# Optimization experiments

Hardware: AMD Instinct MI355X
Metric: run time of the kernel (lower is better)

## Reference

```python
import jax, jax.numpy as jnp
import numpy as np

N, P, S, ENT = 256, 4, 40, 60
E = 1 + P + S + ENT          # 105 graph nodes (query + paras + sents + ents)
D = 1024                     # input_dim == hidden_dim
H, T = 8, 3                  # gnn heads, edge types
DH = D // H                  # per-head output dim
NEG = -1e30


def setup_inputs() -> dict:
    key = jax.random.key(0)
    ks = jax.random.split(key, 12)
    f = lambda k, sh, s: jax.random.normal(k, sh, jnp.float32) * s
    return {
        "query_vec": f(ks[0], (N, D), 1.0),
        "para_state": f(ks[1], (N, P, D), 1.0),
        "sent_state": f(ks[2], (N, S, D), 1.0),
        "ent_state": f(ks[3], (N, ENT, D), 1.0),
        "para_mask": jax.random.randint(ks[4], (N, P), 0, 2).astype(jnp.float32),
        "sent_mask": jax.random.randint(ks[5], (N, S), 0, 2).astype(jnp.float32),
        "ent_mask": jax.random.randint(ks[6], (N, ENT), 0, 2).astype(jnp.float32),
        "adj": jax.random.randint(ks[7], (N, E, E), 0, T + 1).astype(jnp.int32),
        "W": f(ks[8], (H, T, D, DH), 0.05),        # per head/edge-type projection
        "a": f(ks[9], (H, T, 2 * DH), 0.05),       # GAT attention vector [a1;a2]
        "qW1": f(ks[10], (H, T, D, 2 * DH), 0.05), # query-gate layer 1
        "qW2": f(ks[11], (H, T, 2 * DH, 2 * DH), 0.05),  # query-gate layer 2
    }


def _graph_block(x, query_vec, node_mask, adj, W, a, qW1, qW2):
    # x: [N,E,D], node_mask: [N,E,1], adj: [N,E,E] int (0 = no edge, 1..T = edge type)
    # per head/edge-type projections: [H,T,N,E,DH]
    h = jnp.einsum('ned,htdk->htnek', x, W)
    # query-conditioned gate (q_attn=True): sigmoid(relu(q @ W1) @ W2) -> [H,T,N,2DH]
    g = jax.nn.sigmoid(jnp.einsum('htnk,htkm->htnm',
                                  jax.nn.relu(jnp.einsum('nd,htdk->htnk', query_vec, qW1)),
                                  qW2))
    # decomposed GAT score: score[i,j] = lrelu((g1*h_i)@a1 + (g2*h_j)@a2)
    a1, a2 = a[..., :DH], a[..., DH:]
    f1 = jnp.einsum('htnek,htnk->htne', h, g[..., :DH] * a1[:, :, None, :])
    f2 = jnp.einsum('htnek,htnk->htne', h, g[..., DH:] * a2[:, :, None, :])
    score = jax.nn.leaky_relu(f1[..., :, None] + f2[..., None, :], 0.2)  # [H,T,N,E,E]
    # accumulate only where adj matches the edge type (i+1)
    etype = (jnp.arange(T, dtype=adj.dtype) + 1)[None, :, None, None, None]
    scores = jnp.sum(jnp.where(adj[None, None] == etype, score, 0.0), axis=1)  # [H,N,E,E]
    scores = jnp.where(adj[None] > 0, scores, NEG)
    coefs = jax.nn.softmax(scores, axis=-1)                 # [H,N,E,E]
    # original uses the last edge-type projection, node-masked, for aggregation
    h_last = h[:, -1] * node_mask[None]                     # [H,N,E,DH]
    out = jnp.einsum('hnij,hnjd->hnid', coefs, h_last)      # [H,N,E,DH]
    out = jnp.transpose(out, (1, 2, 0, 3)).reshape(x.shape[0], E, H * DH)
    out = jax.nn.relu(out)                                  # dropout p=0 in eval
    return out + x                                          # residual (identity align)


def reference(query_vec, para_state, sent_state, ent_state,
              para_mask, sent_mask, ent_mask, adj, W, a, qW1, qW2):
    x = jnp.concatenate([query_vec[:, None, :], para_state, sent_state, ent_state], axis=1)  # [N,E,D]
    node_mask = jnp.concatenate(
        [jnp.ones((x.shape[0], 1), x.dtype), para_mask, sent_mask, ent_mask], axis=-1)[..., None]  # [N,E,1]
    graph_state = _graph_block(x, query_vec, node_mask, adj, W, a, qW1, qW2)  # [N,E,D]
    return graph_state
```

## Files before the change

kernel.cpp:

```cpp
#include <hip/hip_runtime.h>
#include <stdint.h>


typedef unsigned short u16;
typedef __bf16 bf16;
typedef __bf16 bf16x8 __attribute__((ext_vector_type(8)));
typedef float f32x4 __attribute__((ext_vector_type(4)));

#define N_ 256
#define E_ 105
#define D_ 1024
#define H_ 8
#define DH_ 128
#define NE_ 26880

__device__ __forceinline__ u16 f2b(float f) { bf16 h = (bf16)f; return __builtin_bit_cast(u16, h); }
__device__ __forceinline__ float b2f(u16 u) { bf16 h = __builtin_bit_cast(bf16, u); return (float)h; }

#define AS1 __attribute__((address_space(1)))
#define AS3 __attribute__((address_space(3)))

__device__ __forceinline__ void load16_lds(const void* g, void* l) {
  __builtin_amdgcn_global_load_lds((AS1 void*)(unsigned long long)(uintptr_t)g,
                                   (AS3 void*)l, 16, 0, 0);
}

__device__ __forceinline__ void gemm128(u16* lds, const u16* A, const u16* B, int K,
                                        int lda, int ldb, f32x4 (&acc)[4][4]) {
  u16* lA = lds;
  u16* lB = lds + 8192;
  const int tid  = threadIdx.x;
  const int lane = tid & 63;
  const int wave = tid >> 6;
  const int ln15 = lane & 15;
  const int lq   = lane >> 4;
  const int wRow = (wave >> 1) * 64;
  const int wCol = (wave & 1) * 64;

  const int iters = K >> 6;
  for (int kt = 0; kt < iters; ++kt) {
    const char* Ab = (const char*)A + kt * 128;
    const char* Bb = (const char*)B + kt * 128;
#pragma unroll
    for (int m = 0; m < 4; ++m) {
      int ci  = m * 256 + tid;
      int row = ci >> 3;
      int g   = (ci & 7) ^ (row & 7);
      char* dstA = (char*)lA + m * 4096 + wave * 1024;
      char* dstB = (char*)lB + m * 4096 + wave * 1024;
      load16_lds(Ab + (long)row * ((long)lda * 2) + g * 16, dstA);
      load16_lds(Bb + (long)row * ((long)ldb * 2) + g * 16, dstB);
    }
    __syncthreads();
#pragma unroll
    for (int ks = 0; ks < 2; ++ks) {
      const int cc = ks * 4 + lq;
      bf16x8 af[4], bfv[4];
#pragma unroll
      for (int i = 0; i < 4; ++i) {
        int r = wRow + i * 16 + ln15;
        af[i] = *(const bf16x8*)&lA[r * 64 + ((cc ^ (r & 7)) << 3)];
        int c = wCol + i * 16 + ln15;
        bfv[i] = *(const bf16x8*)&lB[c * 64 + ((cc ^ (c & 7)) << 3)];
      }
#pragma unroll
      for (int i = 0; i < 4; ++i)
#pragma unroll
        for (int j = 0; j < 4; ++j)
          acc[i][j] = __builtin_amdgcn_mfma_f32_16x16x32_bf16(af[i], bfv[j], acc[i][j], 0, 0, 0);
    }
    __syncthreads();
  }
}

__device__ __forceinline__ void zero_acc(f32x4 (&acc)[4][4]) {
  f32x4 z = {0.f, 0.f, 0.f, 0.f};
#pragma unroll
  for (int i = 0; i < 4; ++i)
#pragma unroll
    for (int j = 0; j < 4; ++j) acc[i][j] = z;
}

__global__ __launch_bounds__(256) void k_cast(const float* src, u16* dst, long n) {
  long i = ((long)blockIdx.x * 256 + threadIdx.x) * 4;
  if (i >= n) return;
  float4 v = *(const float4*)(src + i);
  ushort4 o;
  o.x = f2b(v.x); o.y = f2b(v.y); o.z = f2b(v.z); o.w = f2b(v.w);
  *(ushort4*)(dst + i) = o;
}

__global__ __launch_bounds__(256) void k_build(const float* q, const float* para,
                                               const float* sent, const float* ent,
                                               const float* pm, const float* sm,
                                               const float* em, u16* x, float* nmask) {
  long idx = (long)blockIdx.x * 256 + threadIdx.x;
  if (idx >= (long)NE_ * 128) return;
  int ne = (int)(idx >> 7), dc = (int)(idx & 127);
  int n = ne / E_, e = ne - n * E_;
  const float* src;
  if (e == 0)      src = q + (long)n * D_;
  else if (e < 5)  src = para + (long)(n * 4 + (e - 1)) * D_;
  else if (e < 45) src = sent + (long)(n * 40 + (e - 5)) * D_;
  else             src = ent + (long)(n * 60 + (e - 45)) * D_;
  float4 v0 = *(const float4*)(src + dc * 8);
  float4 v1 = *(const float4*)(src + dc * 8 + 4);
  uint4 o;
  o.x = (unsigned)f2b(v0.x) | ((unsigned)f2b(v0.y) << 16);
  o.y = (unsigned)f2b(v0.z) | ((unsigned)f2b(v0.w) << 16);
  o.z = (unsigned)f2b(v1.x) | ((unsigned)f2b(v1.y) << 16);
  o.w = (unsigned)f2b(v1.z) | ((unsigned)f2b(v1.w) << 16);
  *(uint4*)(x + (long)ne * D_ + dc * 8) = o;
  if (dc == 0) {
    float mv;
    if (e == 0)      mv = 1.f;
    else if (e < 5)  mv = pm[n * 4 + e - 1];
    else if (e < 45) mv = sm[n * 40 + e - 5];
    else             mv = em[n * 60 + e - 45];
    nmask[ne] = mv;
  }
}

__global__ __launch_bounds__(256) void k_tr(const float* src, u16* dst, int R, int C,
                                            long sStr, long dStr) {
  __shared__ u16 t[32][33];
  const int bz = blockIdx.y;
  const int tilesC = C >> 5;
  const int tr = (blockIdx.x / tilesC) << 5;
  const int tc = (blockIdx.x % tilesC) << 5;
  const int lr = threadIdx.x >> 5;
  const int lc = threadIdx.x & 31;
#pragma unroll
  for (int i = 0; i < 4; ++i)
    t[lr + i * 8][lc] = f2b(src[bz * sStr + (long)(tr + lr + i * 8) * C + tc + lc]);
  __syncthreads();
#pragma unroll
  for (int i = 0; i < 4; ++i)
    dst[bz * dStr + (long)(tc + lr + i * 8) * R + tr + lc] = t[lc][lr + i * 8];
}

__global__ __launch_bounds__(256) void k_qw1(const u16* x, const u16* qW1t, u16* r_bf) {
  __shared__ u16 shm[16384];
  const int bx = blockIdx.x;
  const int ht = bx >> 2, nt = (bx >> 1) & 1, mt = bx & 1;
  f32x4 acc[4][4];
  zero_acc(acc);
  gemm128(shm, x + (long)nt * 128 * (E_ * D_), qW1t + ((long)ht * 256 + mt * 128) * D_,
          1024, E_ * D_, 1024, acc);
  const int tid = threadIdx.x, lane = tid & 63, wave = tid >> 6;
  const int ln15 = lane & 15, lq = lane >> 4;
  const int wRow = (wave >> 1) * 64, wCol = (wave & 1) * 64;
#pragma unroll
  for (int rt = 0; rt < 4; ++rt)
#pragma unroll
    for (int ct = 0; ct < 4; ++ct)
#pragma unroll
      for (int rg = 0; rg < 4; ++rg) {
        int n = nt * 128 + wRow + rt * 16 + lq * 4 + rg;
        int m = mt * 128 + wCol + ct * 16 + ln15;
        float v = acc[rt][ct][rg];
        if (v < 0.f) v = 0.f;
        r_bf[((long)ht * 256 + n) * 256 + m] = f2b(v);
      }
}

__global__ __launch_bounds__(256) void k_qw2(const u16* r_bf, const u16* qW2t, const float* a,
                                             u16* ga) {
  __shared__ u16 shm[16384];
  const int bx = blockIdx.x;
  const int ht = bx >> 2, nt = (bx >> 1) & 1, mt = bx & 1;
  f32x4 acc[4][4];
  zero_acc(acc);
  gemm128(shm, r_bf + ((long)ht * 256 + nt * 128) * 256, qW2t + ((long)ht * 256 + mt * 128) * 256,
          256, 256, 256, acc);
  const int tid = threadIdx.x, lane = tid & 63, wave = tid >> 6;
  const int ln15 = lane & 15, lq = lane >> 4;
  const int wRow = (wave >> 1) * 64, wCol = (wave & 1) * 64;
#pragma unroll
  for (int rt = 0; rt < 4; ++rt)
#pragma unroll
    for (int ct = 0; ct < 4; ++ct)
#pragma unroll
      for (int rg = 0; rg < 4; ++rg) {
        int n = nt * 128 + wRow + rt * 16 + lq * 4 + rg;
        int m = mt * 128 + wCol + ct * 16 + ln15;
        float v = acc[rt][ct][rg];
        float sig = 1.f / (1.f + __expf(-v));
        float gv = sig * a[ht * 256 + m];
        int s = m >> 7, kk = m & 127;
        ga[(((long)ht * 2 + s) * 256 + n) * 128 + kk] = f2b(gv);
      }
}

__global__ __launch_bounds__(256) void k_w12(const u16* ga, const u16* Wb, u16* w12) {
  __shared__ u16 shm[16384];
  const int bx = blockIdx.x;
  const int c = bx >> 4, r2 = bx & 15;
  const int nt = r2 >> 3, dt = r2 & 7;
  const int ht = c >> 1;
  f32x4 acc[4][4];
  zero_acc(acc);
  gemm128(shm, ga + ((long)c * 256 + nt * 128) * 128, Wb + (long)ht * 131072 + dt * 128 * 128,
          128, 128, 128, acc);
  const int tid = threadIdx.x, lane = tid & 63, wave = tid >> 6;
  const int ln15 = lane & 15, lq = lane >> 4;
  const int wRow = (wave >> 1) * 64, wCol = (wave & 1) * 64;
#pragma unroll
  for (int rt = 0; rt < 4; ++rt)
#pragma unroll
    for (int ct = 0; ct < 4; ++ct)
#pragma unroll
      for (int rg = 0; rg < 4; ++rg) {
        int n = nt * 128 + wRow + rt * 16 + lq * 4 + rg;
        int d = dt * 128 + wCol + ct * 16 + ln15;
        w12[((long)n * 48 + c) * 1024 + d] = f2b(acc[rt][ct][rg]);
      }
}

__global__ __launch_bounds__(256) void k_f(const u16* x, const u16* w12, float* F) {
  __shared__ u16 shm[16384];
  const int n = blockIdx.x;
  f32x4 acc[4][4];
  zero_acc(acc);
  gemm128(shm, x + (long)n * E_ * D_, w12 + (long)n * 48 * 1024, 1024, 1024, 1024, acc);
  const int tid = threadIdx.x, lane = tid & 63, wave = tid >> 6;
  const int ln15 = lane & 15, lq = lane >> 4;
  const int wRow = (wave >> 1) * 64, wCol = (wave & 1) * 64;
#pragma unroll
  for (int rt = 0; rt < 4; ++rt)
#pragma unroll
    for (int ct = 0; ct < 4; ++ct)
#pragma unroll
      for (int rg = 0; rg < 4; ++rg) {
        int e = wRow + rt * 16 + lq * 4 + rg;
        int c = wCol + ct * 16 + ln15;
        if (e < 105 && c < 48) F[((long)n * 48 + c) * 105 + e] = acc[rt][ct][rg];
      }
}

__global__ __launch_bounds__(256) void k_h(const u16* x, const u16* Wt, const float* nmask,
                                           float* out) {
  __shared__ u16 shm[16384];
  const int bx = blockIdx.x;
  const int h = bx / 210;
  const int ne0 = (bx % 210) * 128;
  f32x4 acc[4][4];
  zero_acc(acc);
  gemm128(shm, x + (long)ne0 * D_, Wt + (long)h * DH_ * D_, 1024, 1024, 1024, acc);
  const int tid = threadIdx.x, lane = tid & 63, wave = tid >> 6;
  const int ln15 = lane & 15, lq = lane >> 4;
  const int wRow = (wave >> 1) * 64, wCol = (wave & 1) * 64;
#pragma unroll
  for (int rt = 0; rt < 4; ++rt)
#pragma unroll
    for (int ct = 0; ct < 4; ++ct)
#pragma unroll
      for (int rg = 0; rg < 4; ++rg) {
        int nel = wRow + rt * 16 + lq * 4 + rg;
        int k   = wCol + ct * 16 + ln15;
        shm[k * 128 + (nel ^ ((k & 15) << 3))] = f2b(acc[rt][ct][rg]);
      }
  __syncthreads();
  char* ob = (char*)out;
  for (int it = tid; it < 16384; it += 256) {
    int k = it >> 7, nel = it & 127;
    int ne = ne0 + nel;
    int n = ne / 105;
    int j = ne - n * 105;
    int t = k * 224 + j * 2;
    long gb = ((long)(n * 105 + (t >> 9)) << 12) + ((long)h << 9) + (t & 511);
    u16 v = shm[k * 128 + (nel ^ ((k & 15) << 3))];
    float mv = nmask[ne];
    *(u16*)(ob + gb) = (mv != 0.f) ? v : (u16)0;
    if (j == 104) {
#pragma unroll
      for (int p = 1; p <= 7; ++p) {
        int tp = t + p * 2;
        long gp = ((long)(n * 105 + (tp >> 9)) << 12) + ((long)h << 9) + (tp & 511);
        *(u16*)(ob + gp) = 0;
      }
    }
  }
}

__global__ __launch_bounds__(256) void k_attn(const float* F, const int* adj, const u16* x,
                                              float* out) {
  const int h = blockIdx.x >> 8;
  const int n = blockIdx.x & 255;
  __shared__ u16 cb[112 * 128];
  __shared__ float f1s[3][112];
  __shared__ float f2s[3][112];
  const int tid = threadIdx.x;
  const int lane = tid & 63, wave = tid >> 6;

  for (int i = tid; i < 630; i += 256) {
    int t = i / 210;
    int rm = i - t * 210;
    int s = rm / 105;
    int e = rm - s * 105;
    float v = F[((long)n * 48 + (h * 3 + t) * 2 + s) * 105 + e];
    if (s == 0) f1s[t][e] = v; else f2s[t][e] = v;
  }
  {
    unsigned* cbz = (unsigned*)cb;
    for (int i = tid; i < 112 * 64; i += 256) cbz[i] = 0;
  }
  __syncthreads();

  {
    const int* abase = adj + (long)n * (E_ * E_);
    const int g  = lane >> 4;
    const int lg = lane & 15;
    float f2r[3][7];
#pragma unroll
    for (int m = 0; m < 7; ++m) {
      int j = lg + m * 16;
      bool jv = j < 105;
#pragma unroll
      for (int t = 0; t < 3; ++t) f2r[t][m] = jv ? f2s[t][j] : 0.f;
    }
    for (int it = 0; it < 7; ++it) {
      int i = it * 16 + wave * 4 + g;
      bool iv = i < 105;
      int ir = iv ? i : 0;
      int av[7];
#pragma unroll
      for (int m = 0; m < 7; ++m) {
        int j = lg + m * 16;
        av[m] = (iv && j < 105) ? abase[ir * E_ + j] : 0;
      }
      float f11 = f1s[0][ir], f12 = f1s[1][ir], f13 = f1s[2][ir];
      float s[7];
#pragma unroll
      for (int m = 0; m < 7; ++m) {
        int a_ = av[m];
        float f1v = (a_ == 1) ? f11 : ((a_ == 2) ? f12 : f13);
        float f2v = (a_ == 1) ? f2r[0][m] : ((a_ == 2) ? f2r[1][m] : f2r[2][m]);
        float sv = f1v + f2v;
        sv = (sv < 0.f) ? 0.2f * sv : sv;
        s[m] = (a_ > 0) ? sv : -1e30f;
      }
      float mm = s[0];
#pragma unroll
      for (int m = 1; m < 7; ++m) mm = fmaxf(mm, s[m]);
#pragma unroll
      for (int d = 1; d < 16; d <<= 1) mm = fmaxf(mm, __shfl_xor(mm, d));
      float e[7];
      float sum = 0.f;
#pragma unroll
      for (int m = 0; m < 7; ++m) {
        int j = lg + m * 16;
        e[m] = (j < 105) ? __expf(s[m] - mm) : 0.f;
        sum += e[m];
      }
#pragma unroll
      for (int d = 1; d < 16; d <<= 1) sum += __shfl_xor(sum, d);
      float inv = 1.f / sum;
      if (iv) {
        const int rsw = i & 15;
#pragma unroll
        for (int m = 0; m < 7; ++m) {
          int j = lg + m * 16;
          if (j < 105)
            cb[i * 128 + ((((j >> 3) ^ rsw) << 3) + (j & 7))] = f2b(e[m] * inv);
        }
      }
    }
  }
  __syncthreads();

  const char* hb = (const char*)out + (((long)n * 105) << 12) + ((long)h << 9);
  const int ln15 = lane & 15, lq = lane >> 4;
  const int nmt = (wave < 3) ? 2 : 1;
  f32x4 acc[2][8];
  {
    f32x4 z = {0.f, 0.f, 0.f, 0.f};
#pragma unroll
    for (int a_ = 0; a_ < 2; ++a_)
#pragma unroll
      for (int b_ = 0; b_ < 8; ++b_) acc[a_][b_] = z;
  }
#pragma unroll
  for (int ks = 0; ks < 4; ++ks) {
    const int cc = ks * 4 + lq;
    const int ccb = (cc < 14) ? cc : 0;
    bf16x8 bfr[8];
#pragma unroll
    for (int jn = 0; jn < 8; ++jn) {
      int k = jn * 16 + ln15;
      int t = k * 224 + ccb * 16;
      bfr[jn] = *(const bf16x8*)(hb + ((long)(t >> 9) << 12) + (t & 511));
    }
#pragma unroll
    for (int im = 0; im < 2; ++im) {
      if (im < nmt) {
        int i = (wave + im * 4) * 16 + ln15;
        bf16x8 af = *(const bf16x8*)&cb[i * 128 + ((cc ^ (i & 15)) << 3)];
#pragma unroll
        for (int jn = 0; jn < 8; ++jn)
          acc[im][jn] = __builtin_amdgcn_mfma_f32_16x16x32_bf16(af, bfr[jn], acc[im][jn], 0, 0, 0);
      }
    }
  }
  __syncthreads();

  float* sf = (float*)cb;
#pragma unroll
  for (int pass = 0; pass < 2; ++pass) {
    const int rbase = pass * 54;
    const int rcnt  = pass ? 51 : 54;
    for (int im = 0; im < nmt; ++im)
#pragma unroll
      for (int jn = 0; jn < 8; ++jn)
#pragma unroll
        for (int rg = 0; rg < 4; ++rg) {
          int i = (wave + im * 4) * 16 + lq * 4 + rg;
          if (i >= rbase && i < rbase + rcnt && i < 105) {
            int k = jn * 16 + ln15;
            float v = acc[im][jn][rg];
            sf[(i - rbase) * 132 + k] = v < 0.f ? 0.f : v;
          }
        }
    __syncthreads();
    for (int c = tid; c < rcnt * 32; c += 256) {
      int r = c >> 5, k4 = (c & 31) << 2;
      int i = rbase + r;
      float4 v = *(const float4*)&sf[r * 132 + k4];
      long xb = ((long)(n * E_ + i)) * D_ + h * DH_ + k4;
      ushort4 xv = *(const ushort4*)&x[xb];
      v.x += b2f(xv.x); v.y += b2f(xv.y); v.z += b2f(xv.z); v.w += b2f(xv.w);
      *(float4*)&out[xb] = v;
    }
    if (pass == 0) __syncthreads();
  }
}

extern "C" void kernel_launch(void* const* d_in, const int* in_sizes, int n_in,
                              void* d_out, int out_size, void* d_ws, size_t ws_size,
                              hipStream_t stream) {
  const float* q    = (const float*)d_in[0];
  const float* para = (const float*)d_in[1];
  const float* sent = (const float*)d_in[2];
  const float* ent  = (const float*)d_in[3];
  const float* pm   = (const float*)d_in[4];
  const float* sm   = (const float*)d_in[5];
  const float* em   = (const float*)d_in[6];
  const int*   adj  = (const int*)d_in[7];
  const float* W    = (const float*)d_in[8];
  const float* a    = (const float*)d_in[9];
  const float* qW1  = (const float*)d_in[10];
  const float* qW2  = (const float*)d_in[11];
  float* out = (float*)d_out;
  char* ws = (char*)d_ws;

  u16*   x     = (u16*)(ws);
  float* nmask = (float*)(ws + 55050240);
  u16*   Wb    = (u16*)(ws + 55682048);
  u16*   Wt    = (u16*)(ws + 61973504);
  u16*   qW1t  = (u16*)(ws + 64070656);
  u16*   qW2t  = (u16*)(ws + 76653568);
  u16*   r_bf  = (u16*)(ws + 79799296);
  u16*   ga    = (u16*)(ws + 82945024);
  u16*   w12   = (u16*)(ws + 86090752);
  float* F     = (float*)(ws + 111420416);

  k_build<<<13440, 256, 0, stream>>>(q, para, sent, ent, pm, sm, em, x, nmask);
  k_cast<<<3072, 256, 0, stream>>>(W, Wb, 3145728);
  k_tr<<<dim3(256, 24), 256, 0, stream>>>(qW1, qW1t, 1024, 256, 262144, 262144);
  k_tr<<<dim3(64, 24), 256, 0, stream>>>(qW2, qW2t, 256, 256, 65536, 65536);
  k_tr<<<dim3(128, 8), 256, 0, stream>>>(W + 262144, Wt, 1024, 128, 393216, 131072);
  k_qw1<<<96, 256, 0, stream>>>(x, qW1t, r_bf);
  k_qw2<<<96, 256, 0, stream>>>(r_bf, qW2t, a, ga);
  k_w12<<<768, 256, 0, stream>>>(ga, Wb, w12);
  k_f<<<256, 256, 0, stream>>>(x, w12, F);
  k_h<<<1680, 256, 0, stream>>>(x, Wt, nmask, out);
  k_attn<<<2048, 256, 0, stream>>>(F, adj, x, out);
}
```

Measured before the change: 661.0 us.

## Merge prep kernels into one launch, coalesce k_h stores, prefetch adj, raise MFMA priority

Folds the build, cast and three transpose kernels into one k_prep launch that dispatches on block index, cutting four kernel launches and their tail gaps. The k_h scatter store now loops over output positions in linear order, so consecutive threads write adjacent addresses and padding is zeroed by the owning block. In k_attn the next row's adjacency values are loaded one iteration ahead to hide global latency, and s_setprio is raised around the MFMA loop. The restructured k_h loop scans the full padded range for each graph touched, which adds index arithmetic and idle threads.

Result: slower. 678.8 us (+2.7%).

```diff
diff --git a/kernel.cpp b/kernel.cpp
--- a/kernel.cpp
+++ b/kernel.cpp
@@ -81,55 +81,14 @@
     for (int j = 0; j < 4; ++j) acc[i][j] = z;
 }
 
-__global__ __launch_bounds__(256) void k_cast(const float* src, u16* dst, long n) {
-  long i = ((long)blockIdx.x * 256 + threadIdx.x) * 4;
-  if (i >= n) return;
-  float4 v = *(const float4*)(src + i);
-  ushort4 o;
-  o.x = f2b(v.x); o.y = f2b(v.y); o.z = f2b(v.z); o.w = f2b(v.w);
-  *(ushort4*)(dst + i) = o;
-}
-
-__global__ __launch_bounds__(256) void k_build(const float* q, const float* para,
-                                               const float* sent, const float* ent,
-                                               const float* pm, const float* sm,
-                                               const float* em, u16* x, float* nmask) {
-  long idx = (long)blockIdx.x * 256 + threadIdx.x;
-  if (idx >= (long)NE_ * 128) return;
-  int ne = (int)(idx >> 7), dc = (int)(idx & 127);
-  int n = ne / E_, e = ne - n * E_;
-  const float* src;
-  if (e == 0)      src = q + (long)n * D_;
-  else if (e < 5)  src = para + (long)(n * 4 + (e - 1)) * D_;
-  else if (e < 45) src = sent + (long)(n * 40 + (e - 5)) * D_;
-  else             src = ent + (long)(n * 60 + (e - 45)) * D_;
-  float4 v0 = *(const float4*)(src + dc * 8);
-  float4 v1 = *(const float4*)(src + dc * 8 + 4);
-  uint4 o;
-  o.x = (unsigned)f2b(v0.x) | ((unsigned)f2b(v0.y) << 16);
-  o.y = (unsigned)f2b(v0.z) | ((unsigned)f2b(v0.w) << 16);
-  o.z = (unsigned)f2b(v1.x) | ((unsigned)f2b(v1.y) << 16);
-  o.w = (unsigned)f2b(v1.z) | ((unsigned)f2b(v1.w) << 16);
-  *(uint4*)(x + (long)ne * D_ + dc * 8) = o;
-  if (dc == 0) {
-    float mv;
-    if (e == 0)      mv = 1.f;
-    else if (e < 5)  mv = pm[n * 4 + e - 1];
-    else if (e < 45) mv = sm[n * 40 + e - 5];
-    else             mv = em[n * 60 + e - 45];
-    nmask[ne] = mv;
-  }
-}
-
-__global__ __launch_bounds__(256) void k_tr(const float* src, u16* dst, int R, int C,
-                                            long sStr, long dStr) {
-  __shared__ u16 t[32][33];
-  const int bz = blockIdx.y;
+__device__ __forceinline__ void tr_tile(const float* src, u16* dst, int R, int C,
+                                        long sStr, long dStr, int bz, int bxy,
+                                        u16 (*t)[33], int tid) {
   const int tilesC = C >> 5;
-  const int tr = (blockIdx.x / tilesC) << 5;
-  const int tc = (blockIdx.x % tilesC) << 5;
-  const int lr = threadIdx.x >> 5;
-  const int lc = threadIdx.x & 31;
+  const int tr = (bxy / tilesC) << 5;
+  const int tc = (bxy % tilesC) << 5;
+  const int lr = tid >> 5;
+  const int lc = tid & 31;
 #pragma unroll
   for (int i = 0; i < 4; ++i)
     t[lr + i * 8][lc] = f2b(src[bz * sStr + (long)(tr + lr + i * 8) * C + tc + lc]);
@@ -137,6 +96,60 @@
 #pragma unroll
   for (int i = 0; i < 4; ++i)
     dst[bz * dStr + (long)(tc + lr + i * 8) * R + tr + lc] = t[lc][lr + i * 8];
+}
+
+__global__ __launch_bounds__(256) void k_prep(const float* q, const float* para,
+                                              const float* sent, const float* ent,
+                                              const float* pm, const float* sm,
+                                              const float* em, u16* x, float* nmask,
+                                              const float* W, u16* Wb,
+                                              const float* qW1, u16* qW1t,
+                                              const float* qW2, u16* qW2t,
+                                              u16* Wt) {
+  __shared__ u16 t[32][33];
+  const int b = blockIdx.x;
+  const int tid = threadIdx.x;
+  if (b < 13440) {
+    long idx = (long)b * 256 + tid;
+    int ne = (int)(idx >> 7), dc = (int)(idx & 127);
+    int n = ne / E_, e = ne - n * E_;
+    const float* src;
+    if (e == 0)      src = q + (long)n * D_;
+    else if (e < 5)  src = para + (long)(n * 4 + (e - 1)) * D_;
+    else if (e < 45) src = sent + (long)(n * 40 + (e - 5)) * D_;
+    else             src = ent + (long)(n * 60 + (e - 45)) * D_;
+    float4 v0 = *(const float4*)(src + dc * 8);
+    float4 v1 = *(const float4*)(src + dc * 8 + 4);
+    uint4 o;
+    o.x = (unsigned)f2b(v0.x) | ((unsigned)f2b(v0.y) << 16);
+    o.y = (unsigned)f2b(v0.z) | ((unsigned)f2b(v0.w) << 16);
+    o.z = (unsigned)f2b(v1.x) | ((unsigned)f2b(v1.y) << 16);
+    o.w = (unsigned)f2b(v1.z) | ((unsigned)f2b(v1.w) << 16);
+    *(uint4*)(x + (long)ne * D_ + dc * 8) = o;
+    if (dc == 0) {
+      float mv;
+      if (e == 0)      mv = 1.f;
+      else if (e < 5)  mv = pm[n * 4 + e - 1];
+      else if (e < 45) mv = sm[n * 40 + e - 5];
+      else             mv = em[n * 60 + e - 45];
+      nmask[ne] = mv;
+    }
+  } else if (b < 16512) {
+    long i = ((long)(b - 13440) * 256 + tid) * 4;
+    float4 v = *(const float4*)(W + i);
+    ushort4 o;
+    o.x = f2b(v.x); o.y = f2b(v.y); o.z = f2b(v.z); o.w = f2b(v.w);
+    *(ushort4*)(Wb + i) = o;
+  } else if (b < 22656) {
+    int idx = b - 16512;
+    tr_tile(qW1, qW1t, 1024, 256, 262144, 262144, idx / 256, idx % 256, t, tid);
+  } else if (b < 24192) {
+    int idx = b - 22656;
+    tr_tile(qW2, qW2t, 256, 256, 65536, 65536, idx / 64, idx % 64, t, tid);
+  } else {
+    int idx = b - 24192;
+    tr_tile(W + 262144, Wt, 1024, 128, 393216, 131072, idx / 128, idx % 128, t, tid);
+  }
 }
 
 __global__ __launch_bounds__(256) void k_qw1(const u16* x, const u16* qW1t, u16* r_bf) {
@@ -262,22 +275,29 @@
       }
   __syncthreads();
   char* ob = (char*)out;
-  for (int it = tid; it < 16384; it += 256) {
-    int k = it >> 7, nel = it & 127;
-    int ne = ne0 + nel;
-    int n = ne / 105;
-    int j = ne - n * 105;
-    int t = k * 224 + j * 2;
-    long gb = ((long)(n * 105 + (t >> 9)) << 12) + ((long)h << 9) + (t & 511);
-    u16 v = shm[k * 128 + (nel ^ ((k & 15) << 3))];
-    float mv = nmask[ne];
-    *(u16*)(ob + gb) = (mv != 0.f) ? v : (u16)0;
-    if (j == 104) {
-#pragma unroll
-      for (int p = 1; p <= 7; ++p) {
-        int tp = t + p * 2;
-        long gp = ((long)(n * 105 + (tp >> 9)) << 12) + ((long)h << 9) + (tp & 511);
-        *(u16*)(ob + gp) = 0;
+  const int nStart = ne0 / 105;
+  const int nEnd   = (ne0 + 127) / 105;
+  for (int n = nStart; n <= nEnd; ++n) {
+    const long tb = (((long)n * 105) << 12) + ((long)h << 9);
+    const int pe = n * 105 + 104;
+    const bool ownPad = (pe >= ne0) && (pe < ne0 + 128);
+    for (int t2 = tid; t2 < 14336; t2 += 256) {
+      int c = t2 >> 10;
+      int r = t2 & 1023;
+      int k = r >> 3, e = r & 7;
+      int j = c * 8 + e;
+      int t = t2 * 2;
+      long gb = tb + (long)(t >> 9) * 4096 + (t & 511);
+      if (j < 105) {
+        int ne = n * 105 + j;
+        if (ne >= ne0 && ne < ne0 + 128) {
+          int nel = ne - ne0;
+          u16 v = shm[k * 128 + (nel ^ ((k & 15) << 3))];
+          float mv = nmask[ne];
+          *(u16*)(ob + gb) = (mv != 0.f) ? v : (u16)0;
+        }
+      } else if (ownPad) {
+        *(u16*)(ob + gb) = 0;
       }
     }
   }
@@ -319,21 +339,36 @@
 #pragma unroll
       for (int t = 0; t < 3; ++t) f2r[t][m] = jv ? f2s[t][j] : 0.f;
     }
+    int avc[7];
+    {
+      int i0 = wave * 4 + g;
+#pragma unroll
+      for (int m = 0; m < 7; ++m) {
+        int j = lg + m * 16;
+        avc[m] = (j < 105) ? abase[i0 * E_ + j] : 0;
+      }
+    }
+#pragma unroll
     for (int it = 0; it < 7; ++it) {
       int i = it * 16 + wave * 4 + g;
       bool iv = i < 105;
       int ir = iv ? i : 0;
-      int av[7];
-#pragma unroll
-      for (int m = 0; m < 7; ++m) {
-        int j = lg + m * 16;
-        av[m] = (iv && j < 105) ? abase[ir * E_ + j] : 0;
+      int avn[7];
+      if (it < 6) {
+        int in_ = i + 16;
+        bool ivn = in_ < 105;
+        int irn = ivn ? in_ : 0;
+#pragma unroll
+        for (int m = 0; m < 7; ++m) {
+          int j = lg + m * 16;
+          avn[m] = (ivn && j < 105) ? abase[irn * E_ + j] : 0;
+        }
       }
       float f11 = f1s[0][ir], f12 = f1s[1][ir], f13 = f1s[2][ir];
       float s[7];
 #pragma unroll
       for (int m = 0; m < 7; ++m) {
-        int a_ = av[m];
+        int a_ = avc[m];
         float f1v = (a_ == 1) ? f11 : ((a_ == 2) ? f12 : f13);
         float f2v = (a_ == 1) ? f2r[0][m] : ((a_ == 2) ? f2r[1][m] : f2r[2][m]);
         float sv = f1v + f2v;
@@ -364,6 +399,10 @@
           if (j < 105)
             cb[i * 128 + ((((j >> 3) ^ rsw) << 3) + (j & 7))] = f2b(e[m] * inv);
         }
+      }
+      if (it < 6) {
+#pragma unroll
+        for (int m = 0; m < 7; ++m) avc[m] = avn[m];
       }
     }
   }
@@ -388,9 +427,9 @@
 #pragma unroll
     for (int jn = 0; jn < 8; ++jn) {
       int k = jn * 16 + ln15;
-      int t = k * 224 + ccb * 16;
-      bfr[jn] = *(const bf16x8*)(hb + ((long)(t >> 9) << 12) + (t & 511));
-    }
+      bfr[jn] = *(const bf16x8*)(hb + (long)(ccb * 4 + (k >> 5)) * 4096 + (k & 31) * 16);
+    }
+    __builtin_amdgcn_s_setprio(1);
 #pragma unroll
     for (int im = 0; im < 2; ++im) {
       if (im < nmt) {
@@ -401,6 +440,7 @@
           acc[im][jn] = __builtin_amdgcn_mfma_f32_16x16x32_bf16(af, bfr[jn], acc[im][jn], 0, 0, 0);
       }
     }
+    __builtin_amdgcn_s_setprio(0);
   }
   __syncthreads();
 
@@ -464,11 +504,8 @@
   u16*   w12   = (u16*)(ws + 86090752);
   float* F     = (float*)(ws + 111420416);
 
-  k_build<<<13440, 256, 0, stream>>>(q, para, sent, ent, pm, sm, em, x, nmask);
-  k_cast<<<3072, 256, 0, stream>>>(W, Wb, 3145728);
-  k_tr<<<dim3(256, 24), 256, 0, stream>>>(qW1, qW1t, 1024, 256, 262144, 262144);
-  k_tr<<<dim3(64, 24), 256, 0, stream>>>(qW2, qW2t, 256, 256, 65536, 65536);
-  k_tr<<<dim3(128, 8), 256, 0, stream>>>(W + 262144, Wt, 1024, 128, 393216, 131072);
+  k_prep<<<25216, 256, 0, stream>>>(q, para, sent, ent, pm, sm, em, x, nmask,
+                                    W, Wb, qW1, qW1t, qW2, qW2t, Wt);
   k_qw1<<<96, 256, 0, stream>>>(x, qW1t, r_bf);
   k_qw2<<<96, 256, 0, stream>>>(r_bf, qW2t, a, ga);
   k_w12<<<768, 256, 0, stream>>>(ga, Wb, w12);
```
